# Performance work log

Hardware: AMD Instinct MI355X
Metric: run time of the kernel (lower is better)

The kernel has to match this reference:

```python
import jax, jax.numpy as jnp
import numpy as np

# ---- module hyperparameters (from init_kwargs) ----
B, C, T = 4, 512, 400
K = 31            # kernel_size
STRIDE = 1
WP = 3            # weight_precision -> WP-1 = 2 paired memristor arrays
# DacAdcHardwareSettings
IN_BITS = 8
OUT_PREC = 8
OUT_RANGE = 10
VMAX = 0.6
CUR_SCALE = 8020.0
DAC_SCALE = 1.0 / 2 ** (IN_BITS - 1)
DAC_MIN, DAC_MAX = -(2 ** (IN_BITS - 1)), 2 ** (IN_BITS - 1)
ADC_SCALE = 1.0 / 2 ** OUT_PREC
ADC_MIN, ADC_MAX = -(2 ** (OUT_PREC + OUT_RANGE - 1)), 2 ** (OUT_PREC + OUT_RANGE - 1)
# memristor noise model constants
KBT = 1.380649e-23 * 300.0
BW = 1e-8
E = float(np.exp(1.0))
EPS = 1e-12
INPUT_FACTOR = 1.0
OUTPUT_FACTOR = 1.0


def fake_quant(x, scale, qmin, qmax):
    # torch.fake_quantize_per_tensor_affine with zero_point=0, STE gradient inside range
    q = jnp.round(x / scale)
    qc = jnp.clip(q, qmin, qmax) * scale
    mask = (q >= qmin) & (q <= qmax)
    return jnp.where(mask, x + jax.lax.stop_gradient(qc - x), jax.lax.stop_gradient(qc))


def polyval_asc(coeffs, x):
    # coefficients in ascending degree order (as in poly_mul); Horner over static length
    res = jnp.zeros_like(x)
    for c in coeffs[::-1]:
        res = res * x + c
    return res


def setup_inputs() -> dict:
    key = jax.random.key(0)
    k1, k2, k3, k4, k5 = jax.random.split(key, 5)
    x = jax.random.normal(k1, (B, C, T), dtype=jnp.float32)
    poly_low = jax.random.normal(k2, (WP - 1, 2, 7), dtype=jnp.float32)   # [bit, pos/neg, low_degree]
    poly_high = jax.random.normal(k3, (WP - 1, 2, 6), dtype=jnp.float32)  # [bit, pos/neg, high_degree]
    r = jax.random.uniform(k4, (WP - 1, 2, C, K), dtype=jnp.float32)      # blend factor per cell
    bias = jax.random.normal(k5, (C,), dtype=jnp.float32)
    return {"x": x, "poly_low": poly_low, "poly_high": poly_high, "r": r, "bias": bias}


def reference(x, poly_low, poly_high, r, bias):
    # x: [B, C, T]
    pad = K - 1  # 'same' padding, stride 1
    pl, pr = pad // 2, pad - pad // 2
    xp = jnp.pad(x * INPUT_FACTOR, ((0, 0), (0, 0), (pl, pr)))  # zeros padding mode
    # DAC: fake quantize input, scale to hardware voltage
    v = fake_quant(xp, DAC_SCALE, DAC_MIN, DAC_MAX) * VMAX
    t_out = (T + pad - K) // STRIDE + 1
    idx = jnp.arange(t_out)[:, None] * STRIDE + jnp.arange(K)   # [T_out, K]
    w = v[:, :, idx]                                            # [B, C, T_out, K]
    w = jnp.transpose(w, (0, 2, 1, 3))                          # [B, T_out, C, K] == [...B, A=C, I=K]
    key = jax.random.key(42)
    out = jnp.zeros((B, t_out, C), dtype=x.dtype)
    for i in range(WP - 1):
        bit = WP - 2 - i  # memristors[i] carries bit (WP-2-i), per init_from_conv_quant
        pair = jnp.zeros((B, t_out, C), dtype=x.dtype)
        for s in range(2):  # 0 = pos array, 1 = neg array
            low = polyval_asc(poly_low[i, s], w)
            high = polyval_asc(poly_high[i, s], w)
            rr = r[i, s]  # [C, K], broadcasts over B, T_out (O=1 squeezed)
            raw = low * (1.0 - rr) + high * rr
            johnson = 4.0 * KBT * BW * jnp.abs(raw / (jnp.abs(w) + EPS))
            shot = 2.0 * E * BW * jnp.abs(raw)
            sigma = jnp.sqrt(johnson + shot)
            key, nk = jax.random.split(key)
            # broadcast_noise_dims=1: one noise sample shared across the batch dim
            noise = jax.random.normal(nk, raw.shape[1:], dtype=raw.dtype)
            cur = jnp.sum(raw + noise * sigma, axis=-1)  # reduce I=K -> [B, T_out, C]
            pair = pair + (cur if s == 0 else -cur)
        # ADC per paired array, weighted by the bit significance
        out = out + fake_quant(pair * CUR_SCALE, ADC_SCALE, ADC_MIN, ADC_MAX) * float(2 ** bit)
    out = out * OUTPUT_FACTOR
    out = jnp.transpose(out, (0, 2, 1)) + bias[None, :, None]   # [B, C, T_out]
    return out
```

## Files before the change

### kernel.cpp

```cpp
#include <hip/hip_runtime.h>
#include <cstdint>

#define C_DIM 512
#define T_DIM 400
#define KW 31
#define TOUT 400
#define WSROW 432
#define TPB 128
#define PPB 64

static inline uint32_t h_rotl32(uint32_t x, int d){ return (x<<d)|(x>>(32-d)); }

static void h_threefry2x32(uint32_t k0, uint32_t k1, uint32_t x0, uint32_t x1,
                           uint32_t* o0, uint32_t* o1){
  uint32_t ks2 = k0 ^ k1 ^ 0x1BD11BDAu;
  uint32_t ks[3] = {k0, k1, ks2};
  const int rotA[4] = {13,15,26,6};
  const int rotB[4] = {17,29,16,24};
  uint32_t v0 = x0 + k0, v1 = x1 + k1;
  for (int r = 0; r < 5; ++r){
    const int* rot = (r & 1) ? rotB : rotA;
    for (int q = 0; q < 4; ++q){
      v0 += v1; v1 = h_rotl32(v1, rot[q]); v1 ^= v0;
    }
    v0 += ks[(r+1)%3];
    v1 += ks[(r+2)%3] + (uint32_t)(r+1);
  }
  *o0 = v0; *o1 = v1;
}

template<int R>
__device__ __forceinline__ void tfr4(uint32_t v0[4], uint32_t v1[4]){
  #pragma unroll
  for (int n = 0; n < 4; ++n){
    v0[n] += v1[n];
    v1[n] = (v1[n] << R) | (v1[n] >> (32 - R));
    v1[n] ^= v0[n];
  }
}

__device__ __forceinline__ void tfinj4(uint32_t v0[4], uint32_t v1[4],
                                       const uint32_t a[4], const uint32_t b[4],
                                       uint32_t cadd){
  #pragma unroll
  for (int n = 0; n < 4; ++n){ v0[n] += a[n]; v1[n] += b[n] + cadd; }
}

__device__ __forceinline__ void threefry_xor4(const uint32_t ka[4], const uint32_t kb[4],
                                              uint32_t j, uint32_t out[4]){
  uint32_t ks2[4], v0[4], v1[4];
  #pragma unroll
  for (int n = 0; n < 4; ++n){
    ks2[n] = ka[n] ^ kb[n] ^ 0x1BD11BDAu;
    v0[n] = ka[n];
    v1[n] = j + kb[n];
  }
  tfr4<13>(v0,v1); tfr4<15>(v0,v1); tfr4<26>(v0,v1); tfr4<6>(v0,v1);
  tfinj4(v0,v1,kb,ks2,1u);
  tfr4<17>(v0,v1); tfr4<29>(v0,v1); tfr4<16>(v0,v1); tfr4<24>(v0,v1);
  tfinj4(v0,v1,ks2,ka,2u);
  tfr4<13>(v0,v1); tfr4<15>(v0,v1); tfr4<26>(v0,v1); tfr4<6>(v0,v1);
  tfinj4(v0,v1,ka,kb,3u);
  tfr4<17>(v0,v1); tfr4<29>(v0,v1); tfr4<16>(v0,v1); tfr4<24>(v0,v1);
  tfinj4(v0,v1,kb,ks2,4u);
  tfr4<13>(v0,v1); tfr4<15>(v0,v1); tfr4<26>(v0,v1); tfr4<6>(v0,v1);
  tfinj4(v0,v1,ks2,ka,5u);
  #pragma unroll
  for (int n = 0; n < 4; ++n) out[n] = v0[n] ^ v1[n];
}

__device__ __forceinline__ float erfinv_fast(float x){
  float w = -0.69314718f * __builtin_amdgcn_logf((1.0f - x) * (1.0f + x));
  float p;
  if (w < 5.0f){
    w = w - 2.5f;
    p =              2.81022636e-08f;
    p = fmaf(p, w,   3.43273939e-07f);
    p = fmaf(p, w,  -3.5233877e-06f);
    p = fmaf(p, w,  -4.39150654e-06f);
    p = fmaf(p, w,   0.00021858087f);
    p = fmaf(p, w,  -0.00125372503f);
    p = fmaf(p, w,  -0.00417768164f);
    p = fmaf(p, w,   0.246640727f);
    p = fmaf(p, w,   1.50140941f);
  } else {
    w = __builtin_amdgcn_sqrtf(w) - 3.0f;
    p =             -0.000200214257f;
    p = fmaf(p, w,   0.000100950558f);
    p = fmaf(p, w,   0.00134934322f);
    p = fmaf(p, w,  -0.00367342844f);
    p = fmaf(p, w,   0.00573950773f);
    p = fmaf(p, w,  -0.0076224613f);
    p = fmaf(p, w,   0.00943887047f);
    p = fmaf(p, w,   1.00167406f);
    p = fmaf(p, w,   2.83297682f);
  }
  return p * x;
}

__global__ __launch_bounds__(256) void dac_prepass(
    const float* __restrict__ x, uint2* __restrict__ wsq)
{
  const int m = blockIdx.x * 256 + threadIdx.x;
  const int c  = m / WSROW;
  const int tp = m - c * WSROW;
  const int time = tp - 15;
  const bool inb = (time >= 0) && (time < T_DIM);
  uint32_t qi[4];
  #pragma unroll
  for (int b = 0; b < 4; ++b){
    float xv = inb ? x[(b * C_DIM + c) * T_DIM + time] : 0.0f;
    float q = rintf(xv * 128.0f);
    q = fminf(fmaxf(q, -128.0f), 128.0f);
    qi[b] = (uint32_t)((int)q + 128);
  }
  wsq[m] = make_uint2(qi[0] | (qi[1] << 16), qi[2] | (qi[3] << 16));
}

template<bool USE_WS>
__global__ __launch_bounds__(TPB) void memristor_main(
    const float* __restrict__ x,
    const float* __restrict__ poly_low,
    const float* __restrict__ poly_high,
    const float* __restrict__ r,
    const float* __restrict__ bias,
    const uint2* __restrict__ wsq,
    float* __restrict__ out,
    uint32_t nk0a, uint32_t nk0b, uint32_t nk1a, uint32_t nk1b,
    uint32_t nk2a, uint32_t nk2b, uint32_t nk3a, uint32_t nk3b)
{
  __shared__ __align__(16) float lut[257][12];

  const int tid = threadIdx.x;

  for (int qi = tid; qi < 257; qi += TPB){
    const float q = (float)(qi - 128);
    const float w = (q * 0.0078125f) * 0.6f;
    #pragma unroll
    for (int is = 0; is < 4; ++is){
      const float* pl = poly_low  + is * 7;
      const float* ph = poly_high + is * 6;
      float lo = pl[6];
      lo = fmaf(lo, w, pl[5]); lo = fmaf(lo, w, pl[4]); lo = fmaf(lo, w, pl[3]);
      lo = fmaf(lo, w, pl[2]); lo = fmaf(lo, w, pl[1]); lo = fmaf(lo, w, pl[0]);
      float hi = ph[5];
      hi = fmaf(hi, w, ph[4]); hi = fmaf(hi, w, ph[3]); hi = fmaf(hi, w, ph[2]);
      hi = fmaf(hi, w, ph[1]); hi = fmaf(hi, w, ph[0]);
      lut[qi][is * 2]     = lo;
      lut[qi][is * 2 + 1] = hi - lo;
    }
    const float jf = fmaf(1.6567788e-28f,
                          __builtin_amdgcn_rcpf(fabsf(w) + 1e-12f),
                          5.4365637e-08f);
    lut[qi][8] = __builtin_amdgcn_sqrtf(jf);
  }
  __syncthreads();

  const int h = tid & 1;
  const int p = tid >> 1;
  const int gid = blockIdx.x * PPB + p;
  const int c = gid / TOUT;
  const int t = gid - c * TOUT;
  const int k0 = h ? 16 : 0;

  const uint32_t ka[4] = {nk0a, nk1a, nk2a, nk3a};
  const uint32_t kb[4] = {nk0b, nk1b, nk2b, nk3b};
  const uint32_t jbase = (uint32_t)((t * C_DIM + c) * KW);

  float acc[4][4];
  #pragma unroll
  for (int b = 0; b < 4; ++b)
    #pragma unroll
    for (int is = 0; is < 4; ++is) acc[b][is] = 0.0f;

  auto body = [&](int k){
    uint32_t qi[4];
    if (USE_WS){
      const uint2 ld = wsq[c * WSROW + t + k];
      qi[0] = ld.x & 0xFFFFu; qi[1] = ld.x >> 16;
      qi[2] = ld.y & 0xFFFFu; qi[3] = ld.y >> 16;
    } else {
      const int time = t + k - 15;
      const bool inb = (time >= 0) && (time < T_DIM);
      #pragma unroll
      for (int b = 0; b < 4; ++b){
        float xv = inb ? x[(b * C_DIM + c) * T_DIM + time] : 0.0f;
        float q = rintf(xv * 128.0f);
        q = fminf(fmaxf(q, -128.0f), 128.0f);
        qi[b] = (uint32_t)((int)q + 128);
      }
    }

    uint32_t bits[4];
    threefry_xor4(ka, kb, jbase + (uint32_t)k, bits);

    float noise[4];
    #pragma unroll
    for (int is = 0; is < 4; ++is){
      const float u1 = __uint_as_float((bits[is] >> 9) | 0x3f800000u) - 1.0f;
      const float uu = fmaxf(-0.99999994f, fmaf(u1, 2.0f, -0.99999994f));
      noise[is] = 1.41421356f * erfinv_fast(uu);
    }

    float rr[4];
    #pragma unroll
    for (int is = 0; is < 4; ++is)
      rr[is] = r[(is * C_DIM + c) * KW + k];

    #pragma unroll
    for (int b = 0; b < 4; ++b){
      const float* row = lut[qi[b]];
      const float4 A = *(const float4*)(row);
      const float4 Bv = *(const float4*)(row + 4);
      const float sj = row[8];
      {
        const float raw = fmaf(A.y, rr[0], A.x);
        const float s = __builtin_amdgcn_sqrtf(fabsf(raw));
        acc[b][0] = fmaf(noise[0] * sj, s, acc[b][0] + raw);
      }
      {
        const float raw = fmaf(A.w, rr[1], A.z);
        const float s = __builtin_amdgcn_sqrtf(fabsf(raw));
        acc[b][1] = fmaf(noise[1] * sj, s, acc[b][1] + raw);
      }
      {
        const float raw = fmaf(Bv.y, rr[2], Bv.x);
        const float s = __builtin_amdgcn_sqrtf(fabsf(raw));
        acc[b][2] = fmaf(noise[2] * sj, s, acc[b][2] + raw);
      }
      {
        const float raw = fmaf(Bv.w, rr[3], Bv.z);
        const float s = __builtin_amdgcn_sqrtf(fabsf(raw));
        acc[b][3] = fmaf(noise[3] * sj, s, acc[b][3] + raw);
      }
    }
  };

  for (int kk = 0; kk < 15; ++kk) body(k0 + kk);
  if (h == 0) body(15);

  float tot[4][4];
  #pragma unroll
  for (int b = 0; b < 4; ++b)
    #pragma unroll
    for (int is = 0; is < 4; ++is)
      tot[b][is] = acc[b][is] + __shfl_xor(acc[b][is], 1);

  if (h == 0){
    const float bv = bias[c];
    #pragma unroll
    for (int b = 0; b < 4; ++b){
      float o = 0.0f;
      #pragma unroll
      for (int i = 0; i < 2; ++i){
        const float pair = tot[b][i*2+0] - tot[b][i*2+1];
        float q = rintf((pair * 8020.0f) * 256.0f);
        q = fminf(fmaxf(q, -131072.0f), 131072.0f);
        o += (q * 0.00390625f) * ((i == 0) ? 2.0f : 1.0f);
      }
      out[(b * C_DIM + c) * TOUT + t] = o + bv;
    }
  }
}

extern "C" void kernel_launch(void* const* d_in, const int* in_sizes, int n_in,
                              void* d_out, int out_size, void* d_ws, size_t ws_size,
                              hipStream_t stream) {
  const float* x         = (const float*)d_in[0];
  const float* poly_low  = (const float*)d_in[1];
  const float* poly_high = (const float*)d_in[2];
  const float* r         = (const float*)d_in[3];
  const float* bias      = (const float*)d_in[4];
  float* out             = (float*)d_out;

  uint32_t ck0 = 0u, ck1 = 42u;
  uint32_t nk[4][2];
  for (int n = 0; n < 4; ++n){
    uint32_t a0, a1, b0, b1;
    h_threefry2x32(ck0, ck1, 0u, 0u, &a0, &a1);
    h_threefry2x32(ck0, ck1, 0u, 1u, &b0, &b1);
    nk[n][0] = b0; nk[n][1] = b1;
    ck0 = a0; ck1 = a1;
  }

  const size_t ws_needed = (size_t)C_DIM * WSROW * 8;
  const int nblocks = (C_DIM * TOUT) / PPB;

  if (ws_size >= ws_needed){
    uint2* wsq = (uint2*)d_ws;
    hipLaunchKernelGGL(dac_prepass, dim3((C_DIM * WSROW) / 256), dim3(256),
                       0, stream, x, wsq);
    hipLaunchKernelGGL((memristor_main<true>), dim3(nblocks), dim3(TPB), 0, stream,
                       x, poly_low, poly_high, r, bias, wsq, out,
                       nk[0][0], nk[0][1], nk[1][0], nk[1][1],
                       nk[2][0], nk[2][1], nk[3][0], nk[3][1]);
  } else {
    hipLaunchKernelGGL((memristor_main<false>), dim3(nblocks), dim3(TPB), 0, stream,
                       x, poly_low, poly_high, r, bias, (const uint2*)nullptr, out,
                       nk[0][0], nk[0][1], nk[1][0], nk[1][1],
                       nk[2][0], nk[2][1], nk[3][0], nk[3][1]);
  }
}
```

Baseline: 109.8 us.

## Split tap loop across four lanes, interleave r table, precompute LUT byte offsets

Each output point is now handled by four lanes that each take 7-8 kernel taps, reduced with two xor shuffles, in place of two lanes taking 15-16 taps. Blocks grow to 512 threads and 128 points, and the LUT is built in a single pass. A new prepass transposes r into one float4 per (c,k) so the main loop does one vector load instead of four scalar loads. The DAC prepass now stores LUT byte offsets to skip the address multiply. This adds parallelism and shortens the per-thread critical path, at the cost of an extra kernel launch and more shuffle work per output.

```diff
diff --git a/kernel.cpp b/kernel.cpp
--- a/kernel.cpp
+++ b/kernel.cpp
@@ -6,8 +6,14 @@
 #define KW 31
 #define TOUT 400
 #define WSROW 432
-#define TPB 128
-#define PPB 64
+#define TPB 512
+#define PPB 128
+#define ROWB 48
+
+#define WSQ_BYTES (C_DIM * WSROW * 8)
+#define RT_OFF    WSQ_BYTES
+#define RT_BYTES  (C_DIM * KW * 16)
+#define WS_NEEDED (WSQ_BYTES + RT_BYTES)
 
 static inline uint32_t h_rotl32(uint32_t x, int d){ return (x<<d)|(x>>(32-d)); }
 
@@ -106,15 +112,30 @@
   const int tp = m - c * WSROW;
   const int time = tp - 15;
   const bool inb = (time >= 0) && (time < T_DIM);
-  uint32_t qi[4];
+  uint32_t off[4];
   #pragma unroll
   for (int b = 0; b < 4; ++b){
     float xv = inb ? x[(b * C_DIM + c) * T_DIM + time] : 0.0f;
     float q = rintf(xv * 128.0f);
     q = fminf(fmaxf(q, -128.0f), 128.0f);
-    qi[b] = (uint32_t)((int)q + 128);
-  }
-  wsq[m] = make_uint2(qi[0] | (qi[1] << 16), qi[2] | (qi[3] << 16));
+    off[b] = (uint32_t)(((int)q + 128) * ROWB);
+  }
+  wsq[m] = make_uint2(off[0] | (off[1] << 16), off[2] | (off[3] << 16));
+}
+
+__global__ __launch_bounds__(256) void r_prepass(
+    const float* __restrict__ r, float4* __restrict__ rT)
+{
+  const int m = blockIdx.x * 256 + threadIdx.x;
+  if (m >= C_DIM * KW) return;
+  const int c = m / KW;
+  const int k = m - c * KW;
+  float4 v;
+  v.x = r[(0 * C_DIM + c) * KW + k];
+  v.y = r[(1 * C_DIM + c) * KW + k];
+  v.z = r[(2 * C_DIM + c) * KW + k];
+  v.w = r[(3 * C_DIM + c) * KW + k];
+  rT[m] = v;
 }
 
 template<bool USE_WS>
@@ -125,15 +146,17 @@
     const float* __restrict__ r,
     const float* __restrict__ bias,
     const uint2* __restrict__ wsq,
+    const float4* __restrict__ rT,
     float* __restrict__ out,
     uint32_t nk0a, uint32_t nk0b, uint32_t nk1a, uint32_t nk1b,
     uint32_t nk2a, uint32_t nk2b, uint32_t nk3a, uint32_t nk3b)
 {
-  __shared__ __align__(16) float lut[257][12];
+  __shared__ __align__(16) float lut[257 * 12];
 
   const int tid = threadIdx.x;
 
-  for (int qi = tid; qi < 257; qi += TPB){
+  if (tid < 257){
+    const int qi = tid;
     const float q = (float)(qi - 128);
     const float w = (q * 0.0078125f) * 0.6f;
     #pragma unroll
@@ -146,22 +169,23 @@
       float hi = ph[5];
       hi = fmaf(hi, w, ph[4]); hi = fmaf(hi, w, ph[3]); hi = fmaf(hi, w, ph[2]);
       hi = fmaf(hi, w, ph[1]); hi = fmaf(hi, w, ph[0]);
-      lut[qi][is * 2]     = lo;
-      lut[qi][is * 2 + 1] = hi - lo;
+      lut[qi * 12 + is * 2]     = lo;
+      lut[qi * 12 + is * 2 + 1] = hi - lo;
     }
     const float jf = fmaf(1.6567788e-28f,
                           __builtin_amdgcn_rcpf(fabsf(w) + 1e-12f),
                           5.4365637e-08f);
-    lut[qi][8] = __builtin_amdgcn_sqrtf(jf);
+    lut[qi * 12 + 8] = __builtin_amdgcn_sqrtf(jf);
   }
   __syncthreads();
 
-  const int h = tid & 1;
-  const int p = tid >> 1;
+  const int l   = tid & 3;
+  const int p   = tid >> 2;
   const int gid = blockIdx.x * PPB + p;
-  const int c = gid / TOUT;
-  const int t = gid - c * TOUT;
-  const int k0 = h ? 16 : 0;
+  const int c   = gid / TOUT;
+  const int t   = gid - c * TOUT;
+  const int k0  = l * 8;
+  const int kn  = (l == 3) ? 7 : 8;
 
   const uint32_t ka[4] = {nk0a, nk1a, nk2a, nk3a};
   const uint32_t kb[4] = {nk0b, nk1b, nk2b, nk3b};
@@ -173,12 +197,16 @@
     #pragma unroll
     for (int is = 0; is < 4; ++is) acc[b][is] = 0.0f;
 
-  auto body = [&](int k){
-    uint32_t qi[4];
+  for (int kk = 0; kk < kn; ++kk){
+    const int k = k0 + kk;
+
+    uint32_t off[4];
+    float4 rv;
     if (USE_WS){
       const uint2 ld = wsq[c * WSROW + t + k];
-      qi[0] = ld.x & 0xFFFFu; qi[1] = ld.x >> 16;
-      qi[2] = ld.y & 0xFFFFu; qi[3] = ld.y >> 16;
+      off[0] = ld.x & 0xFFFFu; off[1] = ld.x >> 16;
+      off[2] = ld.y & 0xFFFFu; off[3] = ld.y >> 16;
+      rv = rT[c * KW + k];
     } else {
       const int time = t + k - 15;
       const bool inb = (time >= 0) && (time < T_DIM);
@@ -187,8 +215,12 @@
         float xv = inb ? x[(b * C_DIM + c) * T_DIM + time] : 0.0f;
         float q = rintf(xv * 128.0f);
         q = fminf(fmaxf(q, -128.0f), 128.0f);
-        qi[b] = (uint32_t)((int)q + 128);
-      }
+        off[b] = (uint32_t)(((int)q + 128) * ROWB);
+      }
+      rv.x = r[(0 * C_DIM + c) * KW + k];
+      rv.y = r[(1 * C_DIM + c) * KW + k];
+      rv.z = r[(2 * C_DIM + c) * KW + k];
+      rv.w = r[(3 * C_DIM + c) * KW + k];
     }
 
     uint32_t bits[4];
@@ -202,51 +234,47 @@
       noise[is] = 1.41421356f * erfinv_fast(uu);
     }
 
-    float rr[4];
-    #pragma unroll
-    for (int is = 0; is < 4; ++is)
-      rr[is] = r[(is * C_DIM + c) * KW + k];
-
     #pragma unroll
     for (int b = 0; b < 4; ++b){
-      const float* row = lut[qi[b]];
-      const float4 A = *(const float4*)(row);
+      const float* row = (const float*)((const char*)lut + off[b]);
+      const float4 A  = *(const float4*)(row);
       const float4 Bv = *(const float4*)(row + 4);
-      const float sj = row[8];
+      const float sj  = row[8];
       {
-        const float raw = fmaf(A.y, rr[0], A.x);
+        const float raw = fmaf(A.y, rv.x, A.x);
         const float s = __builtin_amdgcn_sqrtf(fabsf(raw));
         acc[b][0] = fmaf(noise[0] * sj, s, acc[b][0] + raw);
       }
       {
-        const float raw = fmaf(A.w, rr[1], A.z);
+        const float raw = fmaf(A.w, rv.y, A.z);
         const float s = __builtin_amdgcn_sqrtf(fabsf(raw));
         acc[b][1] = fmaf(noise[1] * sj, s, acc[b][1] + raw);
       }
       {
-        const float raw = fmaf(Bv.y, rr[2], Bv.x);
+        const float raw = fmaf(Bv.y, rv.z, Bv.x);
         const float s = __builtin_amdgcn_sqrtf(fabsf(raw));
         acc[b][2] = fmaf(noise[2] * sj, s, acc[b][2] + raw);
       }
       {
-        const float raw = fmaf(Bv.w, rr[3], Bv.z);
+        const float raw = fmaf(Bv.w, rv.w, Bv.z);
         const float s = __builtin_amdgcn_sqrtf(fabsf(raw));
         acc[b][3] = fmaf(noise[3] * sj, s, acc[b][3] + raw);
       }
     }
-  };
-
-  for (int kk = 0; kk < 15; ++kk) body(k0 + kk);
-  if (h == 0) body(15);
+  }
 
   float tot[4][4];
   #pragma unroll
   for (int b = 0; b < 4; ++b)
     #pragma unroll
-    for (int is = 0; is < 4; ++is)
-      tot[b][is] = acc[b][is] + __shfl_xor(acc[b][is], 1);
-
-  if (h == 0){
+    for (int is = 0; is < 4; ++is){
+      float v = acc[b][is];
+      v += __shfl_xor(v, 1);
+      v += __shfl_xor(v, 2);
+      tot[b][is] = v;
+    }
+
+  if (l == 0){
     const float bv = bias[c];
     #pragma unroll
     for (int b = 0; b < 4; ++b){
@@ -283,20 +311,23 @@
     ck0 = a0; ck1 = a1;
   }
 
-  const size_t ws_needed = (size_t)C_DIM * WSROW * 8;
   const int nblocks = (C_DIM * TOUT) / PPB;
 
-  if (ws_size >= ws_needed){
-    uint2* wsq = (uint2*)d_ws;
+  if (ws_size >= (size_t)WS_NEEDED){
+    uint2*  wsq = (uint2*)d_ws;
+    float4* rT  = (float4*)((char*)d_ws + RT_OFF);
     hipLaunchKernelGGL(dac_prepass, dim3((C_DIM * WSROW) / 256), dim3(256),
                        0, stream, x, wsq);
+    hipLaunchKernelGGL(r_prepass, dim3((C_DIM * KW + 255) / 256), dim3(256),
+                       0, stream, r, rT);
     hipLaunchKernelGGL((memristor_main<true>), dim3(nblocks), dim3(TPB), 0, stream,
-                       x, poly_low, poly_high, r, bias, wsq, out,
+                       x, poly_low, poly_high, r, bias, wsq, rT, out,
                        nk[0][0], nk[0][1], nk[1][0], nk[1][1],
                        nk[2][0], nk[2][1], nk[3][0], nk[3][1]);
   } else {
     hipLaunchKernelGGL((memristor_main<false>), dim3(nblocks), dim3(TPB), 0, stream,
-                       x, poly_low, poly_high, r, bias, (const uint2*)nullptr, out,
+                       x, poly_low, poly_high, r, bias,
+                       (const uint2*)nullptr, (const float4*)nullptr, out,
                        nk[0][0], nk[0][1], nk[1][0], nk[1][1],
                        nk[2][0], nk[2][1], nk[3][0], nk[3][1]);
   }
```

New measurement: 108.5 us. About the same (-1.2%).
